# Performance work log

Measured on AMD Instinct MI355X. Metric: run time of the kernel, lower is better.

The kernel has to match this reference:

```python
import jax, jax.numpy as jnp
import numpy as np

D_MODEL = 1024
NUM_HEADS = 16
DEPTH = D_MODEL // NUM_HEADS
B, S = 2, 2048


def setup_inputs() -> dict:
    key = jax.random.key(0)
    k1, k2, k3 = jax.random.split(key, 3)
    x = jax.random.normal(k1, (B, S, D_MODEL), dtype=jnp.float32)
    # causal mask: 1.0 where attention is disallowed (upper triangle)
    causal = 1.0 - jnp.tril(jnp.ones((S, S), dtype=jnp.float32))
    mask = causal[None, None, :, :]  # [1,1,S,S]
    w_attn = jax.random.normal(k2, (D_MODEL, 3 * D_MODEL), dtype=jnp.float32) * 0.02
    b_attn = jnp.zeros((3 * D_MODEL,), dtype=jnp.float32)
    w_proj = jax.random.normal(k3, (D_MODEL, D_MODEL), dtype=jnp.float32) * 0.02
    b_proj = jnp.zeros((D_MODEL,), dtype=jnp.float32)
    return {"x": x, "mask": mask, "w_attn": w_attn, "b_attn": b_attn,
            "w_proj": w_proj, "b_proj": b_proj}


def _split_heads(t):
    # [B,S,D] -> [B,H,S,depth]
    b, s, _ = t.shape
    return t.reshape(b, s, NUM_HEADS, DEPTH).transpose(0, 2, 1, 3)


def reference(x, mask, w_attn, b_attn, w_proj, b_proj):
    # QKV projection (Conv1d == pointwise dense over last axis)
    qkv = jnp.einsum('bsd,de->bse', x, w_attn) + b_attn
    q, k, v = jnp.split(qkv, 3, axis=2)
    q, k, v = _split_heads(q), _split_heads(k), _split_heads(v)  # [B,H,S,depth]
    present = jnp.stack([k, v], axis=1)  # [B,2,H,S,depth]
    # scaled dot-product attention (inference: no dropout)
    scores = jnp.einsum('bhqd,bhkd->bhqk', q, k) / jnp.sqrt(
        jnp.asarray(DEPTH, dtype=x.dtype))
    scores = scores + mask * (-1e9)
    attn = jax.nn.softmax(scores, axis=-1)
    out = jnp.einsum('bhqk,bhkd->bhqd', attn, v)
    # merge heads: [B,H,S,depth] -> [B,S,D]
    out = out.transpose(0, 2, 1, 3).reshape(x.shape[0], -1, D_MODEL)
    out = jnp.einsum('bsd,de->bse', out, w_proj) + b_proj
    return out, present
```

## Files before the change

kernel.cpp:

```cpp
#include <hip/hip_runtime.h>
#include <stdint.h>

typedef unsigned short u16;
typedef unsigned int u32;
typedef short bf16x8 __attribute__((ext_vector_type(8)));
typedef float f32x4 __attribute__((ext_vector_type(4)));
typedef float f32x16 __attribute__((ext_vector_type(16)));

#define SEQ 2048
#define NH 16
#define DM 1024
#define DEPTH 64

#define QSCALE 0.18033688f
#define SMAX 16.0f

__device__ __forceinline__ u16 f2bf(float f) {
  union { float f; u32 i; } v; v.f = f;
  u32 x = v.i;
  x += 0x7fffu + ((x >> 16) & 1u);
  return (u16)(x >> 16);
}

__device__ __forceinline__ float fexp2(float x) {
#if __has_builtin(__builtin_amdgcn_exp2f)
  return __builtin_amdgcn_exp2f(x);
#else
  return exp2f(x);
#endif
}

__device__ __forceinline__ u32 cvtpk(float lo, float hi) {
  u32 r;
  asm("v_cvt_pk_bf16_f32 %0, %1, %2" : "=v"(r) : "v"(lo), "v"(hi));
  return r;
}
__device__ __forceinline__ float bflo(u32 w) {
  union { u32 i; float f; } u; u.i = w << 16; return u.f;
}
__device__ __forceinline__ float bfhi(u32 w) {
  union { u32 i; float f; } u; u.i = w & 0xffff0000u; return u.f;
}

__device__ __forceinline__ void gload_lds16(const u16* g, u16* l) {
  __builtin_amdgcn_global_load_lds(
      (const __attribute__((address_space(1))) u32*)g,
      (__attribute__((address_space(3))) u32*)l, 16, 0, 0);
}

__global__ __launch_bounds__(256)
void cvt_bf16(const float* __restrict__ src, u16* __restrict__ dst) {
  int i = (blockIdx.x * 256 + threadIdx.x) * 4;
  float4 v = *(const float4*)(src + i);
  ushort4 o; o.x = f2bf(v.x); o.y = f2bf(v.y); o.z = f2bf(v.z); o.w = f2bf(v.w);
  *(ushort4*)(dst + i) = o;
}

__global__ __launch_bounds__(256)
void cvtT_both(const float* __restrict__ wa, const float* __restrict__ wp,
               u16* __restrict__ dwa, u16* __restrict__ dwp) {
  __shared__ float t[32][33];
  const int tid = threadIdx.x;
  const int bx = blockIdx.x;
  const float* src; u16* dst; int N, n0;
  if (bx < 96) { src = wa; dst = dwa; N = 3 * DM; n0 = bx << 5; }
  else         { src = wp; dst = dwp; N = DM;     n0 = (bx - 96) << 5; }
  const int k0 = blockIdx.y << 5;
  const int K = DM;
  {
    int r = tid >> 3, c4 = (tid & 7) << 2;
    float4 v = *(const float4*)(src + (size_t)(k0 + r) * N + n0 + c4);
    t[r][c4 + 0] = v.x; t[r][c4 + 1] = v.y; t[r][c4 + 2] = v.z; t[r][c4 + 3] = v.w;
  }
  __syncthreads();
  {
    int n = tid >> 3, k4 = (tid & 7) << 2;
    ushort4 o;
    o.x = f2bf(t[k4 + 0][n]); o.y = f2bf(t[k4 + 1][n]);
    o.z = f2bf(t[k4 + 2][n]); o.w = f2bf(t[k4 + 3][n]);
    *(ushort4*)(dst + (size_t)(n0 + n) * K + k0 + k4) = o;
  }
}

__global__ __launch_bounds__(256)
void v_transpose(const float* __restrict__ present, u16* __restrict__ vt) {
  __shared__ float t[64][65];
  const int tid = threadIdx.x;
  const int st = blockIdx.x, bh = blockIdx.y;
  const int b = bh >> 4, h = bh & 15;
  const int s0 = st << 6;
  const float* vsrc = present + (((size_t)((b * 2 + 1) * NH + h)) * SEQ + s0) * DEPTH;
  u16* vdst = vt + ((size_t)(b * NH + h) * DEPTH) * SEQ + s0;
#pragma unroll
  for (int i = 0; i < 4; ++i) {
    int e = tid + (i << 8);
    int r = e >> 4, c = e & 15;
    float4 v = *(const float4*)(vsrc + (size_t)r * DEPTH + (c << 2));
    t[r][(c << 2) + 0] = v.x; t[r][(c << 2) + 1] = v.y;
    t[r][(c << 2) + 2] = v.z; t[r][(c << 2) + 3] = v.w;
  }
  __syncthreads();
#pragma unroll
  for (int i = 0; i < 2; ++i) {
    int e = tid + (i << 8);
    int d = e >> 3, s8 = (e & 7) << 3;
    ushort4 o0, o1;
    o0.x = f2bf(t[s8 + 0][d]); o0.y = f2bf(t[s8 + 1][d]);
    o0.z = f2bf(t[s8 + 2][d]); o0.w = f2bf(t[s8 + 3][d]);
    o1.x = f2bf(t[s8 + 4][d]); o1.y = f2bf(t[s8 + 5][d]);
    o1.z = f2bf(t[s8 + 6][d]); o1.w = f2bf(t[s8 + 7][d]);
    *(ushort4*)(vdst + (size_t)d * SEQ + s8) = o0;
    *(ushort4*)(vdst + (size_t)d * SEQ + s8 + 4) = o1;
  }
}

__global__ __launch_bounds__(256)
void gemm_mfma(const u16* __restrict__ A, const u16* __restrict__ Bt,
               const float* __restrict__ bias, int M, int N, int K, int mode,
               float* __restrict__ outf, u16* __restrict__ qws,
               float* __restrict__ present, u16* __restrict__ kbp)
{
  __shared__ __align__(16) u16 As[128][64];
  __shared__ __align__(16) u16 Bs[128][64];
  const int tid = threadIdx.x;
  const int m0 = blockIdx.y << 7;
  const int n0 = blockIdx.x << 7;
  const int w = tid >> 6, lane = tid & 63;
  const int lane15 = lane & 15, quad = lane >> 4;
  const int wm = (w >> 1) << 6, wn = (w & 1) << 6;

  const int srow = lane >> 3;
  const int sseg = (lane & 7) ^ srow;
  const u16* agbase = A  + (size_t)(m0 + w * 32 + srow) * K + sseg * 8;
  const u16* bgbase = Bt + (size_t)(n0 + w * 32 + srow) * K + sseg * 8;

  const int l7 = lane15 & 7;

  f32x4 acc[4][4] = {};

  for (int k0 = 0; k0 < K; k0 += 64) {
#pragma unroll
    for (int i = 0; i < 4; ++i) {
      gload_lds16(agbase + (size_t)(i * 8) * K + k0, &As[w * 32 + i * 8][0]);
      gload_lds16(bgbase + (size_t)(i * 8) * K + k0, &Bs[w * 32 + i * 8][0]);
    }
    __syncthreads();
#pragma unroll
    for (int ks = 0; ks < 2; ++ks) {
      const int fs = ((ks * 4 + quad) ^ l7) << 3;
      bf16x8 af[4], bfr[4];
#pragma unroll
      for (int tm = 0; tm < 4; ++tm)
        af[tm] = *(const bf16x8*)&As[wm + tm * 16 + lane15][fs];
#pragma unroll
      for (int tn = 0; tn < 4; ++tn)
        bfr[tn] = *(const bf16x8*)&Bs[wn + tn * 16 + lane15][fs];
#pragma unroll
      for (int tm = 0; tm < 4; ++tm)
#pragma unroll
        for (int tn = 0; tn < 4; ++tn)
          acc[tm][tn] = __builtin_amdgcn_mfma_f32_16x16x32_bf16(af[tm], bfr[tn], acc[tm][tn], 0, 0, 0);
    }
    __syncthreads();
  }

#pragma unroll
  for (int tn = 0; tn < 4; ++tn) {
    const int c = n0 + wn + tn * 16 + lane15;
    const float bc = bias[c];
    const int t = c >> 10, cc = c & 1023;
    const int h = cc >> 6, d = cc & 63;
#pragma unroll
    for (int tm = 0; tm < 4; ++tm) {
#pragma unroll
      for (int r = 0; r < 4; ++r) {
        const int m = m0 + wm + tm * 16 + quad * 4 + r;
        const float val = acc[tm][tn][r] + bc;
        if (mode == 1) {
          outf[(size_t)m * N + c] = val;
        } else {
          const int b = m >> 11, s = m & 2047;
          if (t == 0) {
            qws[(((size_t)(b * NH + h) * SEQ) + s) * DEPTH + d] = f2bf(val * QSCALE);
          } else {
            const size_t pidx = (((size_t)((b * 2 + (t - 1)) * NH + h) * SEQ) + s) * DEPTH + d;
            present[pidx] = val;
            if (t == 1)
              kbp[(((size_t)(b * NH + h) * SEQ) + s) * DEPTH + d] = f2bf(val);
          }
        }
      }
    }
  }
}

__global__ __launch_bounds__(256, 4)
void attn_mfma(const u16* __restrict__ qb, const u16* __restrict__ kb,
               const u16* __restrict__ vt, u16* __restrict__ attnb)
{
  __shared__ __align__(16) u16 Ks[2][64][64];
  __shared__ __align__(16) u16 Vs[2][64][64];

  const int tid = threadIdx.x;
  const int w = tid >> 6, lane = tid & 63;
  const int l31 = lane & 31, hi = lane >> 5;
  const int qh = w >> 1, kh = w & 1;
  const int tt = blockIdx.x, bh = blockIdx.y;
  const int b = bh >> 4, h = bh & 15;

  const u16* qbh = qb + ((size_t)(b * NH + h) * SEQ) * DEPTH;
  const u16* kbh = kb + ((size_t)(b * NH + h) * SEQ) * DEPTH;
  const u16* vbh = vt + ((size_t)(b * NH + h) * DEPTH) * SEQ;

  const int srr = lane >> 3;
  const int sseg = (lane & 7) ^ srr;
  const int r0 = w * 16 + srr;
  const int r1 = r0 + 8;
  const int kr0 = (r0 & ~12) | ((r0 & 4) << 1) | ((r0 & 8) >> 1);
  const int kr1 = (r1 & ~12) | ((r1 & 4) << 1) | ((r1 & 8) >> 1);

  const int rbase = kh * 32 + l31;
  const int swz = l31 & 7;

  const int sloc = (tt << 6) + qh * 32 + l31;
  const int nch = tt + 1;

  const int koff0 = ((0 + hi) ^ swz) << 4;
  const int koff1 = ((2 + hi) ^ swz) << 4;
  const int koff2 = ((4 + hi) ^ swz) << 4;
  const int koff3 = ((6 + hi) ^ swz) << 4;
  const int voffA = ((kh * 4 + 0 + hi) ^ swz) << 4;
  const int voffB = ((kh * 4 + 2 + hi) ^ swz) << 4;

  const u16* kgp0 = kbh + (size_t)kr0 * DEPTH + sseg * 8;
  const u16* kgp1 = kbh + (size_t)kr1 * DEPTH + sseg * 8;
  const u16* vgp0 = vbh + (size_t)r0 * SEQ + sseg * 8;
  const u16* vgp1 = vbh + (size_t)r1 * SEQ + sseg * 8;

  gload_lds16(kgp0, &Ks[0][w * 16][0]);
  gload_lds16(kgp1, &Ks[0][w * 16 + 8][0]);
  gload_lds16(vgp0, &Vs[0][w * 16][0]);
  gload_lds16(vgp1, &Vs[0][w * 16 + 8][0]);

  const u16* qrow = qbh + (size_t)sloc * DEPTH + hi * 8;
  bf16x8 qf0 = *(const bf16x8*)(qrow);
  bf16x8 qf1 = *(const bf16x8*)(qrow + 16);
  bf16x8 qf2 = *(const bf16x8*)(qrow + 32);
  bf16x8 qf3 = *(const bf16x8*)(qrow + 48);

  f32x16 accO0 = {};
  f32x16 accO1 = {};
  float L = 0.f;

  __syncthreads();

#pragma unroll 1
  for (int ct = 0; ct < nch; ++ct) {
    const int bb = ct & 1;
    if (ct + 1 < nch) {
      kgp0 += 64 * DEPTH; kgp1 += 64 * DEPTH;
      vgp0 += 64; vgp1 += 64;
      gload_lds16(kgp0, &Ks[bb ^ 1][w * 16][0]);
      gload_lds16(kgp1, &Ks[bb ^ 1][w * 16 + 8][0]);
      gload_lds16(vgp0, &Vs[bb ^ 1][w * 16][0]);
      gload_lds16(vgp1, &Vs[bb ^ 1][w * 16 + 8][0]);
    }
    const bool atdiag = (ct == tt);
    if (!(atdiag && qh == 0 && kh == 1)) {
      const char* kbase = (const char*)&Ks[bb][rbase][0];
      f32x16 sc;
#pragma unroll
      for (int j = 0; j < 16; ++j) sc[j] = -SMAX;
      {
        bf16x8 af0 = *(const bf16x8*)(kbase + koff0);
        sc = __builtin_amdgcn_mfma_f32_32x32x16_bf16(af0, qf0, sc, 0, 0, 0);
        bf16x8 af1 = *(const bf16x8*)(kbase + koff1);
        sc = __builtin_amdgcn_mfma_f32_32x32x16_bf16(af1, qf1, sc, 0, 0, 0);
        bf16x8 af2 = *(const bf16x8*)(kbase + koff2);
        sc = __builtin_amdgcn_mfma_f32_32x32x16_bf16(af2, qf2, sc, 0, 0, 0);
        bf16x8 af3 = *(const bf16x8*)(kbase + koff3);
        sc = __builtin_amdgcn_mfma_f32_32x32x16_bf16(af3, qf3, sc, 0, 0, 0);
      }
      float pe[16];
      if (atdiag && (qh == kh)) {
#pragma unroll
        for (int j = 0; j < 16; ++j) {
          float e = fexp2(sc[j]);
          if ((16 * (j >> 3) + 8 * hi + (j & 7)) > l31) e = 0.f;
          pe[j] = e;
        }
      } else {
#pragma unroll
        for (int j = 0; j < 16; ++j) pe[j] = fexp2(sc[j]);
      }
      const u32 pk0 = cvtpk(pe[0], pe[1]),   pk1 = cvtpk(pe[2], pe[3]);
      const u32 pk2 = cvtpk(pe[4], pe[5]),   pk3 = cvtpk(pe[6], pe[7]);
      const u32 pk4 = cvtpk(pe[8], pe[9]),   pk5 = cvtpk(pe[10], pe[11]);
      const u32 pk6 = cvtpk(pe[12], pe[13]), pk7 = cvtpk(pe[14], pe[15]);
      float l0 = bflo(pk0) + bfhi(pk0);
      float l1 = bflo(pk1) + bfhi(pk1);
      l0 += bflo(pk2) + bfhi(pk2);
      l1 += bflo(pk3) + bfhi(pk3);
      l0 += bflo(pk4) + bfhi(pk4);
      l1 += bflo(pk5) + bfhi(pk5);
      l0 += bflo(pk6) + bfhi(pk6);
      l1 += bflo(pk7) + bfhi(pk7);
      L += l0 + l1;
      union { u32 u[4]; bf16x8 v; } f0, f1;
      f0.u[0] = pk0; f0.u[1] = pk1; f0.u[2] = pk2; f0.u[3] = pk3;
      f1.u[0] = pk4; f1.u[1] = pk5; f1.u[2] = pk6; f1.u[3] = pk7;
      const char* vbase = (const char*)&Vs[bb][l31][0];
      {
        bf16x8 av0 = *(const bf16x8*)(vbase + voffA);
        accO0 = __builtin_amdgcn_mfma_f32_32x32x16_bf16(av0, f0.v, accO0, 0, 0, 0);
        bf16x8 av1 = *(const bf16x8*)(vbase + 4096 + voffA);
        accO1 = __builtin_amdgcn_mfma_f32_32x32x16_bf16(av1, f0.v, accO1, 0, 0, 0);
        bf16x8 av2 = *(const bf16x8*)(vbase + voffB);
        accO0 = __builtin_amdgcn_mfma_f32_32x32x16_bf16(av2, f1.v, accO0, 0, 0, 0);
        bf16x8 av3 = *(const bf16x8*)(vbase + 4096 + voffB);
        accO1 = __builtin_amdgcn_mfma_f32_32x32x16_bf16(av3, f1.v, accO1, 0, 0, 0);
      }
    }
    __syncthreads();
  }

  float Lw = L + __shfl_xor(L, 32);
  float* red  = (float*)&Ks[0][0][0];
  float* redL = (float*)&Vs[0][0][0];
  const int base = qh * 2048 + lane * 4;
  if (kh) {
#pragma unroll
    for (int g = 0; g < 4; ++g) {
      float4 v0 = make_float4(accO0[4 * g], accO0[4 * g + 1], accO0[4 * g + 2], accO0[4 * g + 3]);
      *(float4*)&red[base + g * 256] = v0;
      float4 v1 = make_float4(accO1[4 * g], accO1[4 * g + 1], accO1[4 * g + 2], accO1[4 * g + 3]);
      *(float4*)&red[base + 1024 + g * 256] = v1;
    }
    redL[qh * 64 + lane] = Lw;
  }
  __syncthreads();
  if (!kh) {
    const float li = 1.0f / (Lw + redL[qh * 64 + lane]);
    u16* ob = attnb + ((size_t)(b * SEQ + sloc)) * DM + h * DEPTH;
#pragma unroll
    for (int g = 0; g < 4; ++g) {
      float4 p0 = *(const float4*)&red[base + g * 256];
      ushort4 st0;
      st0.x = f2bf((accO0[4 * g + 0] + p0.x) * li);
      st0.y = f2bf((accO0[4 * g + 1] + p0.y) * li);
      st0.z = f2bf((accO0[4 * g + 2] + p0.z) * li);
      st0.w = f2bf((accO0[4 * g + 3] + p0.w) * li);
      *(ushort4*)(ob + 8 * g + 4 * hi) = st0;
      float4 p1 = *(const float4*)&red[base + 1024 + g * 256];
      ushort4 st1;
      st1.x = f2bf((accO1[4 * g + 0] + p1.x) * li);
      st1.y = f2bf((accO1[4 * g + 1] + p1.y) * li);
      st1.z = f2bf((accO1[4 * g + 2] + p1.z) * li);
      st1.w = f2bf((accO1[4 * g + 3] + p1.w) * li);
      *(ushort4*)(ob + 32 + 8 * g + 4 * hi) = st1;
    }
  }
}

extern "C" void kernel_launch(void* const* d_in, const int* in_sizes, int n_in,
                              void* d_out, int out_size, void* d_ws, size_t ws_size,
                              hipStream_t stream) {
  (void)in_sizes; (void)n_in; (void)out_size; (void)ws_size;
  const float* x      = (const float*)d_in[0];
  const float* w_attn = (const float*)d_in[2];
  const float* b_attn = (const float*)d_in[3];
  const float* w_proj = (const float*)d_in[4];
  const float* b_proj = (const float*)d_in[5];

  float* out     = (float*)d_out;
  float* present = out + (size_t)2 * SEQ * DM;

  u16* qws   = (u16*)d_ws;
  u16* kbp   = qws + (size_t)4194304;
  u16* xb    = kbp + (size_t)4194304;
  u16* vtp   = xb;
  u16* wabT  = xb + (size_t)4194304;
  u16* attnb = wabT;
  u16* wpbT  = wabT + (size_t)4194304;

  cvt_bf16<<<4096, 256, 0, stream>>>(x, xb);
  cvtT_both<<<dim3(128, 32), 256, 0, stream>>>(w_attn, w_proj, wabT, wpbT);

  gemm_mfma<<<dim3(24, 32), 256, 0, stream>>>(xb, wabT, b_attn,
                                              2 * SEQ, 3 * DM, DM, 0,
                                              nullptr, qws, present, kbp);
  v_transpose<<<dim3(32, 32), 256, 0, stream>>>(present, vtp);
  attn_mfma<<<dim3(32, 32), 256, 0, stream>>>(qws, kbp, vtp, attnb);
  gemm_mfma<<<dim3(8, 32), 256, 0, stream>>>(attnb, wpbT, b_proj,
                                             2 * SEQ, DM, DM, 1,
                                             out, nullptr, nullptr, nullptr);
}
```

Baseline: 218.4 us.

## Double-buffer GEMM LDS tiles, remap block IDs across XCDs, raise MFMA priority

The GEMM now keeps two LDS buffers for the A and B tiles and issues the next k-tile's global-to-LDS loads before computing on the current one. This overlaps memory latency with MFMA work and drops one barrier per iteration. Workgroup IDs are remapped so consecutive tiles land on the same XCD, which should improve L2 locality. s_setprio is raised around the MFMA block. The cost is twice the LDS per block, which can lower occupancy. The remap assumes the workgroup count is divisible by 8.

```diff
diff --git a/kernel.cpp b/kernel.cpp
--- a/kernel.cpp
+++ b/kernel.cpp
@@ -120,11 +120,17 @@
                float* __restrict__ outf, u16* __restrict__ qws,
                float* __restrict__ present, u16* __restrict__ kbp)
 {
-  __shared__ __align__(16) u16 As[128][64];
-  __shared__ __align__(16) u16 Bs[128][64];
+  __shared__ __align__(16) u16 As[2][128][64];
+  __shared__ __align__(16) u16 Bs[2][128][64];
   const int tid = threadIdx.x;
-  const int m0 = blockIdx.y << 7;
-  const int n0 = blockIdx.x << 7;
+
+  const u32 nwg = gridDim.x * gridDim.y;
+  const u32 bid0 = blockIdx.y * gridDim.x + blockIdx.x;
+  const u32 cpx = nwg >> 3;
+  const u32 bid = (bid0 & 7) * cpx + (bid0 >> 3);
+  const int m0 = (int)(bid / gridDim.x) << 7;
+  const int n0 = (int)(bid % gridDim.x) << 7;
+
   const int w = tid >> 6, lane = tid & 63;
   const int lane15 = lane & 15, quad = lane >> 4;
   const int wm = (w >> 1) << 6, wn = (w & 1) << 6;
@@ -138,28 +144,42 @@
 
   f32x4 acc[4][4] = {};
 
-  for (int k0 = 0; k0 < K; k0 += 64) {
-#pragma unroll
-    for (int i = 0; i < 4; ++i) {
-      gload_lds16(agbase + (size_t)(i * 8) * K + k0, &As[w * 32 + i * 8][0]);
-      gload_lds16(bgbase + (size_t)(i * 8) * K + k0, &Bs[w * 32 + i * 8][0]);
-    }
-    __syncthreads();
+  const int nk = K >> 6;
+#pragma unroll
+  for (int i = 0; i < 4; ++i) {
+    gload_lds16(agbase + (size_t)(i * 8) * K, &As[0][w * 32 + i * 8][0]);
+    gload_lds16(bgbase + (size_t)(i * 8) * K, &Bs[0][w * 32 + i * 8][0]);
+  }
+  __syncthreads();
+
+#pragma unroll 1
+  for (int kt = 0; kt < nk; ++kt) {
+    const int cur = kt & 1;
+    if (kt + 1 < nk) {
+      const int kn = (kt + 1) << 6;
+#pragma unroll
+      for (int i = 0; i < 4; ++i) {
+        gload_lds16(agbase + (size_t)(i * 8) * K + kn, &As[cur ^ 1][w * 32 + i * 8][0]);
+        gload_lds16(bgbase + (size_t)(i * 8) * K + kn, &Bs[cur ^ 1][w * 32 + i * 8][0]);
+      }
+    }
 #pragma unroll
     for (int ks = 0; ks < 2; ++ks) {
       const int fs = ((ks * 4 + quad) ^ l7) << 3;
       bf16x8 af[4], bfr[4];
 #pragma unroll
       for (int tm = 0; tm < 4; ++tm)
-        af[tm] = *(const bf16x8*)&As[wm + tm * 16 + lane15][fs];
+        af[tm] = *(const bf16x8*)&As[cur][wm + tm * 16 + lane15][fs];
 #pragma unroll
       for (int tn = 0; tn < 4; ++tn)
-        bfr[tn] = *(const bf16x8*)&Bs[wn + tn * 16 + lane15][fs];
+        bfr[tn] = *(const bf16x8*)&Bs[cur][wn + tn * 16 + lane15][fs];
+      __builtin_amdgcn_s_setprio(1);
 #pragma unroll
       for (int tm = 0; tm < 4; ++tm)
 #pragma unroll
         for (int tn = 0; tn < 4; ++tn)
           acc[tm][tn] = __builtin_amdgcn_mfma_f32_16x16x32_bf16(af[tm], bfr[tn], acc[tm][tn], 0, 0, 0);
+      __builtin_amdgcn_s_setprio(0);
     }
     __syncthreads();
   }
```

Result: no change. 222.5 us (+1.9%).
